# Performance work log

Hardware: AMD Instinct MI355X
Metric: run time of the kernel (lower is better)

## Reference

```python
import jax, jax.numpy as jnp
import numpy as np

N_NODES = 50000
N_EDGES = 800000
IN_DIM = 128
HID = 64
OUT = 32
HEADS = 2
NEG_SLOPE = 0.2  # PyG GATConv default


def _gat_layer(x, edge_index, W, a_src, a_dst, b, concat):
    """PyG-style GATConv (add_self_loops=True, eval mode so dropout is a no-op).
    x: [N, F_in], W: [F_in, H*C], a_src/a_dst: [H, C], b: [H*C] or [C].
    """
    N = x.shape[0]
    H, C = a_src.shape
    loops = jnp.arange(N, dtype=edge_index.dtype)
    src = jnp.concatenate([edge_index[0], loops])  # [E+N]
    dst = jnp.concatenate([edge_index[1], loops])

    h = (x @ W).reshape(N, H, C)                   # [N, H, C]
    alpha_src = jnp.sum(h * a_src, axis=-1)        # [N, H]
    alpha_dst = jnp.sum(h * a_dst, axis=-1)        # [N, H]

    e = jax.nn.leaky_relu(alpha_src[src] + alpha_dst[dst], NEG_SLOPE)  # [E+N, H]
    # segment softmax over incoming edges per destination node
    e_max = jax.ops.segment_max(e, dst, num_segments=N)               # [N, H]
    e_exp = jnp.exp(e - e_max[dst])
    denom = jax.ops.segment_sum(e_exp, dst, num_segments=N)           # [N, H]
    alpha = e_exp / denom[dst]                                        # [E+N, H]

    msg = h[src] * alpha[..., None]                                   # [E+N, H, C]
    out = jax.ops.segment_sum(msg, dst, num_segments=N)               # [N, H, C]
    if concat:
        return out.reshape(N, H * C) + b
    return out.mean(axis=1) + b


def setup_inputs() -> dict:
    key = jax.random.key(0)
    ks = jax.random.split(key, 10)
    x = jax.random.normal(ks[0], (N_NODES, IN_DIM), dtype=jnp.float32)
    edge_index = jax.random.randint(ks[1], (2, N_EDGES), 0, N_NODES, dtype=jnp.int64)
    s1 = 1.0 / np.sqrt(IN_DIM)
    s2 = 1.0 / np.sqrt(HEADS * HID)
    return {
        "x": x,
        "edge_index": edge_index,
        "W1": jax.random.normal(ks[2], (IN_DIM, HEADS * HID), dtype=jnp.float32) * s1,
        "a_src1": jax.random.normal(ks[3], (HEADS, HID), dtype=jnp.float32) * s2,
        "a_dst1": jax.random.normal(ks[4], (HEADS, HID), dtype=jnp.float32) * s2,
        "b1": jnp.zeros((HEADS * HID,), dtype=jnp.float32),
        "W2": jax.random.normal(ks[5], (HEADS * HID, OUT), dtype=jnp.float32) * s2,
        "a_src2": jax.random.normal(ks[6], (1, OUT), dtype=jnp.float32) * (1.0 / np.sqrt(OUT)),
        "a_dst2": jax.random.normal(ks[7], (1, OUT), dtype=jnp.float32) * (1.0 / np.sqrt(OUT)),
        "b2": jnp.zeros((OUT,), dtype=jnp.float32),
    }


def reference(x, edge_index, W1, a_src1, a_dst1, b1, W2, a_src2, a_dst2, b2):
    h = _gat_layer(x, edge_index, W1, a_src1, a_dst1, b1, concat=True)   # [N, HEADS*HID]
    h = jax.nn.relu(h)  # dropout is identity in eval mode
    out = _gat_layer(h, edge_index, W2, a_src2, a_dst2, b2, concat=False)  # [N, OUT]
    return out
```

## Files before the change

### kernel.cpp

```cpp
#include <hip/hip_runtime.h>

#define NEG 0.2f

constexpr int NB  = 196;
constexpr int PB  = 4608;
constexpr int EPB = 4096;

using short8 = __attribute__((ext_vector_type(8))) short;
using f32x4  = __attribute__((ext_vector_type(4))) float;

__device__ __forceinline__ ushort f2bf(float f) {
  uint u = __float_as_uint(f);
  return (ushort)((u + 0x7fffu + ((u >> 16) & 1u)) >> 16);
}
__device__ __forceinline__ float bflo(uint u) { return __uint_as_float(u << 16); }
__device__ __forceinline__ float bfhi(uint u) { return __uint_as_float(u & 0xffff0000u); }

__global__ void prep_kernel(const float* __restrict__ W1, ushort* __restrict__ w1t,
                            const float* __restrict__ W2, ushort* __restrict__ w2t,
                            int* __restrict__ bcursor)
{
  const int b = blockIdx.x, t = threadIdx.x;
  if (b < 64) {
    const int idx = b * 256 + t;
    const int n = idx >> 7, k = idx & 127;
    w1t[idx] = f2bf(W1[k * 128 + n]);
  } else {
    for (int i = t; i < 4096; i += 256) {
      const int n = i >> 7, k = i & 127;
      w2t[i] = f2bf(W2[k * 32 + n]);
    }
    if (t < NB) bcursor[t] = 0;
  }
}

__global__ __launch_bounds__(256) void binA_kernel(const int* __restrict__ ei,
                                                   int* __restrict__ bcursor,
                                                   int2* __restrict__ tmp, int E)
{
  __shared__ int cnt[NB];
  __shared__ int base[NB];
  const int t = threadIdx.x;
  const int e0 = blockIdx.x * EPB;
  const int e1 = min(e0 + EPB, E);

  if (t < NB) cnt[t] = 0;
  __syncthreads();
  for (int i = e0 + t; i < e1; i += 256)
    atomicAdd(&cnt[ei[E + i] >> 8], 1);
  __syncthreads();
  if (t < NB) {
    const int c = cnt[t];
    if (c > 0) base[t] = atomicAdd(&bcursor[t], c);
    cnt[t] = 0;
  }
  __syncthreads();
  for (int i = e0 + t; i < e1; i += 256) {
    const int s = ei[i];
    const int d = ei[E + i];
    const int b = d >> 8;
    const int pos = base[b] + atomicAdd(&cnt[b], 1);
    tmp[(size_t)b * PB + pos] = make_int2(s, d);
  }
}

__global__ __launch_bounds__(256) void binB_kernel(const int2* __restrict__ tmp,
                                                   const int* __restrict__ bcursor,
                                                   int2* __restrict__ offs2,
                                                   int* __restrict__ ssrc, int N)
{
  __shared__ int cnt[256];
  __shared__ int cur[256];
  __shared__ int sc[256];
  const int b = blockIdx.x;
  const int t = threadIdx.x;
  const int d0 = b << 8;
  const int beg = b * PB;
  const int cE = bcursor[b];

  cnt[t] = 0;
  __syncthreads();
  for (int i = t; i < cE; i += 256)
    atomicAdd(&cnt[tmp[beg + i].y - d0], 1);
  __syncthreads();
  sc[t] = cnt[t];
  __syncthreads();
  for (int off = 1; off < 256; off <<= 1) {
    int v = (t >= off) ? sc[t - off] : 0;
    __syncthreads();
    sc[t] += v;
    __syncthreads();
  }
  const int ebase = sc[t] - cnt[t];
  cur[t] = ebase;
  const int dst = d0 + t;
  if (dst < N) offs2[dst] = make_int2(beg + ebase, beg + ebase + cnt[t]);
  __syncthreads();
  for (int i = t; i < cE; i += 256) {
    const int2 e = tmp[beg + i];
    const int pos = beg + atomicAdd(&cur[e.y - d0], 1);
    ssrc[pos] = e.x;
  }
}

constexpr int BM1 = 64;

__global__ __launch_bounds__(256, 2) void gemm1_kernel(
    const float* __restrict__ x, const ushort* __restrict__ wtg,
    const float* __restrict__ a_src, const float* __restrict__ a_dst,
    ushort* __restrict__ h, float* __restrict__ asrc, float* __restrict__ adst,
    int N)
{
  __shared__ ushort xs[64][136];
  __shared__ ushort wt[128][136];
  const int t = threadIdx.x;
  const int n0 = blockIdx.x * BM1;

#pragma unroll
  for (int i = 0; i < 8; ++i) {
    const int idx = t + i * 256;
    const int row = idx >> 5;
    const int q   = idx & 31;
    int rn = n0 + row; if (rn >= N) rn = N - 1;
    const float4 v = *(const float4*)(x + (size_t)rn * 128 + q * 4);
    ushort4 o;
    o.x = f2bf(v.x); o.y = f2bf(v.y); o.z = f2bf(v.z); o.w = f2bf(v.w);
    *(ushort4*)&xs[row][q * 4] = o;
  }
#pragma unroll
  for (int i = 0; i < 8; ++i) {
    const int idx = t + i * 256;
    const int nr = idx >> 4;
    const int qq = idx & 15;
    const uint4 v = *(const uint4*)(wtg + (size_t)nr * 128 + qq * 8);
    *(uint4*)&wt[nr][qq * 8] = v;
  }
  __syncthreads();

  const int w   = t >> 6;
  const int l   = t & 63;
  const int c   = l & 15;
  const int g   = l >> 4;
  const int wr0 = w * 16;

  f32x4 acc[8];
#pragma unroll
  for (int nt = 0; nt < 8; ++nt) acc[nt] = {0.f, 0.f, 0.f, 0.f};

#pragma unroll
  for (int kc = 0; kc < 4; ++kc) {
    const int kb = kc * 32 + g * 8;
    const short8 af = *(const short8*)&xs[wr0 + c][kb];
#pragma unroll
    for (int nt = 0; nt < 8; ++nt) {
      const short8 bf = *(const short8*)&wt[nt * 16 + c][kb];
      acc[nt] = __builtin_amdgcn_mfma_f32_16x16x32_bf16(af, bf, acc[nt], 0, 0, 0);
    }
  }

  float pvs[2][4] = {{0.f,0.f,0.f,0.f},{0.f,0.f,0.f,0.f}};
  float pvd[2][4] = {{0.f,0.f,0.f,0.f},{0.f,0.f,0.f,0.f}};
#pragma unroll
  for (int nt = 0; nt < 8; ++nt) {
    const int col = nt * 16 + c;
    const float as = a_src[col];
    const float ad = a_dst[col];
    const int hd = nt >> 2;
#pragma unroll
    for (int r = 0; r < 4; ++r) {
      pvs[hd][r] += acc[nt][r] * as;
      pvd[hd][r] += acc[nt][r] * ad;
    }
  }
#pragma unroll
  for (int nt = 0; nt < 8; ++nt) {
    const int col = nt * 16 + c;
#pragma unroll
    for (int r = 0; r < 4; ++r) {
      const int nn = n0 + wr0 + g * 4 + r;
      if (nn < N) h[(size_t)nn * 128 + col] = f2bf(acc[nt][r]);
    }
  }
#pragma unroll
  for (int hd = 0; hd < 2; ++hd) {
#pragma unroll
    for (int r = 0; r < 4; ++r) {
#pragma unroll
      for (int m = 1; m <= 8; m <<= 1) {
        pvs[hd][r] += __shfl_xor(pvs[hd][r], m, 64);
        pvd[hd][r] += __shfl_xor(pvd[hd][r], m, 64);
      }
    }
  }
  if (c == 0) {
#pragma unroll
    for (int r = 0; r < 4; ++r) {
      const int nn = n0 + wr0 + g * 4 + r;
      if (nn < N) {
        asrc[nn * 2 + 0] = pvs[0][r];
        asrc[nn * 2 + 1] = pvs[1][r];
        adst[nn * 2 + 0] = pvd[0][r];
        adst[nn * 2 + 1] = pvd[1][r];
      }
    }
  }
}

constexpr int BM2 = 64;

__global__ __launch_bounds__(256, 2) void gemm2_kernel(
    const ushort* __restrict__ xb, const ushort* __restrict__ w2t,
    const float* __restrict__ a_src, const float* __restrict__ a_dst,
    ushort* __restrict__ h, float* __restrict__ asrc, float* __restrict__ adst,
    int N)
{
  __shared__ ushort xs[64][136];
  __shared__ ushort wt[32][136];
  const int t = threadIdx.x;
  const int n0 = blockIdx.x * BM2;

#pragma unroll
  for (int i = 0; i < 4; ++i) {
    const int idx = t + i * 256;
    const int row = idx >> 4;
    const int qq  = idx & 15;
    int rn = n0 + row; if (rn >= N) rn = N - 1;
    const uint4 v = *(const uint4*)(xb + (size_t)rn * 128 + qq * 8);
    *(uint4*)&xs[row][qq * 8] = v;
  }
#pragma unroll
  for (int i = 0; i < 2; ++i) {
    const int idx = t + i * 256;
    const int nr = idx >> 4;
    const int qq = idx & 15;
    const uint4 v = *(const uint4*)(w2t + (size_t)nr * 128 + qq * 8);
    *(uint4*)&wt[nr][qq * 8] = v;
  }
  __syncthreads();

  const int w   = t >> 6;
  const int l   = t & 63;
  const int c   = l & 15;
  const int g   = l >> 4;
  const int wr0 = w * 16;

  f32x4 acc[2];
  acc[0] = {0.f, 0.f, 0.f, 0.f};
  acc[1] = {0.f, 0.f, 0.f, 0.f};

#pragma unroll
  for (int kc = 0; kc < 4; ++kc) {
    const int kb = kc * 32 + g * 8;
    const short8 af = *(const short8*)&xs[wr0 + c][kb];
#pragma unroll
    for (int nt = 0; nt < 2; ++nt) {
      const short8 bf = *(const short8*)&wt[nt * 16 + c][kb];
      acc[nt] = __builtin_amdgcn_mfma_f32_16x16x32_bf16(af, bf, acc[nt], 0, 0, 0);
    }
  }

  float pvs[4] = {0.f, 0.f, 0.f, 0.f};
  float pvd[4] = {0.f, 0.f, 0.f, 0.f};
#pragma unroll
  for (int nt = 0; nt < 2; ++nt) {
    const int col = nt * 16 + c;
    const float as = a_src[col];
    const float ad = a_dst[col];
#pragma unroll
    for (int r = 0; r < 4; ++r) {
      pvs[r] += acc[nt][r] * as;
      pvd[r] += acc[nt][r] * ad;
    }
  }
#pragma unroll
  for (int nt = 0; nt < 2; ++nt) {
    const int col = nt * 16 + c;
#pragma unroll
    for (int r = 0; r < 4; ++r) {
      const int nn = n0 + wr0 + g * 4 + r;
      if (nn < N) h[(size_t)nn * 32 + col] = f2bf(acc[nt][r]);
    }
  }
#pragma unroll
  for (int r = 0; r < 4; ++r) {
#pragma unroll
    for (int m = 1; m <= 8; m <<= 1) {
      pvs[r] += __shfl_xor(pvs[r], m, 64);
      pvd[r] += __shfl_xor(pvd[r], m, 64);
    }
  }
  if (c == 0) {
#pragma unroll
    for (int r = 0; r < 4; ++r) {
      const int nn = n0 + wr0 + g * 4 + r;
      if (nn < N) {
        asrc[nn] = pvs[r];
        adst[nn] = pvd[r];
      }
    }
  }
}

__global__ __launch_bounds__(256) void agg1_kernel(
    const int2* __restrict__ offs2, const int* __restrict__ ssrc,
    const ushort* __restrict__ h, const float* __restrict__ asrc,
    const float* __restrict__ adst, const float* __restrict__ b,
    ushort* __restrict__ out, int N)
{
  const int n = (blockIdx.x * 256 + threadIdx.x) >> 6;
  const int lane = threadIdx.x & 63;
  const int sub = lane & 15;
  const int g = lane >> 4;
  const int head = sub >> 3;
  if (n >= N) return;

  const float2 adv = *(const float2*)(adst + 2 * n);
  const float advh = head ? adv.y : adv.x;

  float a0 = 0.f, a1 = 0.f, a2 = 0.f, a3 = 0.f;
  float a4 = 0.f, a5 = 0.f, a6 = 0.f, a7 = 0.f;
  float den = 0.f;

  const int2 be = offs2[n];
  const int beg = be.x, end = be.y;

  for (int i0 = beg + g; i0 < end; i0 += 16) {
    int    si[4];
    bool   vv[4];
    float2 av[4];
    uint4  gi[4];
#pragma unroll
    for (int j = 0; j < 4; ++j) {
      const int i = i0 + 4 * j;
      vv[j] = i < end;
      si[j] = vv[j] ? ssrc[i] : ssrc[i0];
    }
#pragma unroll
    for (int j = 0; j < 4; ++j)
      av[j] = *(const float2*)(asrc + 2 * si[j]);
#pragma unroll
    for (int j = 0; j < 4; ++j)
      gi[j] = *(const uint4*)(h + (size_t)si[j] * 128 + sub * 8);
#pragma unroll
    for (int j = 0; j < 4; ++j) {
      float e = (head ? av[j].y : av[j].x) + advh;
      e = e > 0.f ? e : NEG * e;
      const float w = vv[j] ? __expf(e) : 0.f;
      const uint4 gv = gi[j];
      den += w;
      a0 += w * bflo(gv.x); a1 += w * bfhi(gv.x);
      a2 += w * bflo(gv.y); a3 += w * bfhi(gv.y);
      a4 += w * bflo(gv.z); a5 += w * bfhi(gv.z);
      a6 += w * bflo(gv.w); a7 += w * bfhi(gv.w);
    }
  }

  if (g == 0) {
    const float2 asv = *(const float2*)(asrc + 2 * n);
    float e = (head ? asv.y : asv.x) + advh;
    e = e > 0.f ? e : NEG * e;
    const float w = __expf(e);
    den += w;
    const uint4 gv = *(const uint4*)(h + (size_t)n * 128 + sub * 8);
    a0 += w * bflo(gv.x); a1 += w * bfhi(gv.x);
    a2 += w * bflo(gv.y); a3 += w * bfhi(gv.y);
    a4 += w * bflo(gv.z); a5 += w * bfhi(gv.z);
    a6 += w * bflo(gv.w); a7 += w * bfhi(gv.w);
  }

#pragma unroll
  for (int m = 16; m <= 32; m <<= 1) {
    a0 += __shfl_xor(a0, m, 64); a1 += __shfl_xor(a1, m, 64);
    a2 += __shfl_xor(a2, m, 64); a3 += __shfl_xor(a3, m, 64);
    a4 += __shfl_xor(a4, m, 64); a5 += __shfl_xor(a5, m, 64);
    a6 += __shfl_xor(a6, m, 64); a7 += __shfl_xor(a7, m, 64);
    den += __shfl_xor(den, m, 64);
  }

  if (g == 0) {
    const float4 b0 = *(const float4*)(b + sub * 8);
    const float4 b1 = *(const float4*)(b + sub * 8 + 4);
    const float inv = 1.f / den;
    float r0 = a0 * inv + b0.x, r1 = a1 * inv + b0.y;
    float r2 = a2 * inv + b0.z, r3 = a3 * inv + b0.w;
    float r4 = a4 * inv + b1.x, r5 = a5 * inv + b1.y;
    float r6 = a6 * inv + b1.z, r7 = a7 * inv + b1.w;
    r0 = r0 > 0.f ? r0 : 0.f; r1 = r1 > 0.f ? r1 : 0.f;
    r2 = r2 > 0.f ? r2 : 0.f; r3 = r3 > 0.f ? r3 : 0.f;
    r4 = r4 > 0.f ? r4 : 0.f; r5 = r5 > 0.f ? r5 : 0.f;
    r6 = r6 > 0.f ? r6 : 0.f; r7 = r7 > 0.f ? r7 : 0.f;
    uint4 o;
    o.x = ((uint)f2bf(r1) << 16) | f2bf(r0);
    o.y = ((uint)f2bf(r3) << 16) | f2bf(r2);
    o.z = ((uint)f2bf(r5) << 16) | f2bf(r4);
    o.w = ((uint)f2bf(r7) << 16) | f2bf(r6);
    *(uint4*)(out + (size_t)n * 128 + sub * 8) = o;
  }
}

__global__ __launch_bounds__(256) void agg2_kernel(
    const int2* __restrict__ offs2, const int* __restrict__ ssrc,
    const ushort* __restrict__ h, const float* __restrict__ asrc,
    const float* __restrict__ adst, const float* __restrict__ b,
    float* __restrict__ out, int N)
{
  const int n = (blockIdx.x * 256 + threadIdx.x) >> 6;
  const int lane = threadIdx.x & 63;
  const int g = lane >> 3;
  const int c4 = (lane & 7) << 2;
  if (n >= N) return;

  const float adv = adst[n];
  float4 a = make_float4(0.f, 0.f, 0.f, 0.f);
  float den = 0.f;

  const int2 be = offs2[n];
  const int beg = be.x, end = be.y;

  for (int i0 = beg + g; i0 < end; i0 += 32) {
    int   si[4];
    bool  vv[4];
    float av[4];
    uint2 ui[4];
#pragma unroll
    for (int j = 0; j < 4; ++j) {
      const int i = i0 + 8 * j;
      vv[j] = i < end;
      si[j] = vv[j] ? ssrc[i] : ssrc[i0];
    }
#pragma unroll
    for (int j = 0; j < 4; ++j)
      av[j] = asrc[si[j]];
#pragma unroll
    for (int j = 0; j < 4; ++j)
      ui[j] = *(const uint2*)(h + (size_t)si[j] * 32 + c4);
#pragma unroll
    for (int j = 0; j < 4; ++j) {
      float e = av[j] + adv;
      e = e > 0.f ? e : NEG * e;
      const float w = vv[j] ? __expf(e) : 0.f;
      den += w;
      a.x += w * bflo(ui[j].x);
      a.y += w * bfhi(ui[j].x);
      a.z += w * bflo(ui[j].y);
      a.w += w * bfhi(ui[j].y);
    }
  }

  if (g == 0) {
    float e = asrc[n] + adv;
    e = e > 0.f ? e : NEG * e;
    const float w = __expf(e);
    den += w;
    const uint2 hv = *(const uint2*)(h + (size_t)n * 32 + c4);
    a.x += w * bflo(hv.x); a.y += w * bfhi(hv.x);
    a.z += w * bflo(hv.y); a.w += w * bfhi(hv.y);
  }

#pragma unroll
  for (int m = 8; m <= 32; m <<= 1) {
    a.x += __shfl_xor(a.x, m, 64);
    a.y += __shfl_xor(a.y, m, 64);
    a.z += __shfl_xor(a.z, m, 64);
    a.w += __shfl_xor(a.w, m, 64);
    den += __shfl_xor(den, m, 64);
  }

  if (g == 0) {
    const float4 bv = *(const float4*)(b + c4);
    const float inv = 1.f / den;
    float4 r;
    r.x = a.x * inv + bv.x;
    r.y = a.y * inv + bv.y;
    r.z = a.z * inv + bv.z;
    r.w = a.w * inv + bv.w;
    *(float4*)(out + (size_t)n * 32 + c4) = r;
  }
}

extern "C" void kernel_launch(void* const* d_in, const int* in_sizes, int n_in,
                              void* d_out, int out_size, void* d_ws, size_t ws_size,
                              hipStream_t stream)
{
  const float* x   = (const float*)d_in[0];
  const int*   ei  = (const int*)  d_in[1];
  const float* W1  = (const float*)d_in[2];
  const float* as1 = (const float*)d_in[3];
  const float* ad1 = (const float*)d_in[4];
  const float* b1  = (const float*)d_in[5];
  const float* W2  = (const float*)d_in[6];
  const float* as2 = (const float*)d_in[7];
  const float* ad2 = (const float*)d_in[8];
  const float* b2  = (const float*)d_in[9];

  const int N = in_sizes[0] / 128;
  const int E = in_sizes[1] / 2;
  const size_t PT = (size_t)NB * PB;

  char* p = (char*)d_ws;
  int* bcursor  = (int*)p;               p += (size_t)NB * 4;
  int2* offs2   = (int2*)p;              p += (size_t)N * 8;
  int2* tmp     = (int2*)p;              p += PT * 8;
  int* ssrc     = (int*)p;               p += PT * 4;
  ushort* w1t   = (ushort*)p;            p += (size_t)128 * 128 * 2;
  ushort* w2t   = (ushort*)p;            p += (size_t)32 * 128 * 2;
  ushort* h1    = (ushort*)p;            p += (size_t)N * 128 * 2;
  ushort* out1  = (ushort*)p;            p += (size_t)N * 128 * 2;
  ushort* h2    = (ushort*)p;            p += (size_t)N * 32 * 2;
  float* asrc1  = (float*)p;             p += (size_t)N * 2 * 4;
  float* adst1  = (float*)p;             p += (size_t)N * 2 * 4;
  float* asrc2  = (float*)p;             p += (size_t)N * 4;
  float* adst2  = (float*)p;             p += (size_t)N * 4;
  float* out    = (float*)d_out;

  const int nchunk = (E + EPB - 1) / EPB;

  prep_kernel<<<65, 256, 0, stream>>>(W1, w1t, W2, w2t, bcursor);
  binA_kernel<<<nchunk, 256, 0, stream>>>(ei, bcursor, tmp, E);
  binB_kernel<<<NB, 256, 0, stream>>>(tmp, bcursor, offs2, ssrc, N);

  gemm1_kernel<<<(N + BM1 - 1) / BM1, 256, 0, stream>>>(x, w1t, as1, ad1,
                                                        h1, asrc1, adst1, N);
  agg1_kernel<<<(N * 64 + 255) / 256, 256, 0, stream>>>(offs2, ssrc, h1,
                                                        asrc1, adst1, b1, out1, N);

  gemm2_kernel<<<(N + BM2 - 1) / BM2, 256, 0, stream>>>(out1, w2t, as2, ad2,
                                                        h2, asrc2, adst2, N);
  agg2_kernel<<<(N * 64 + 255) / 256, 256, 0, stream>>>(offs2, ssrc, h2,
                                                        asrc2, adst2, b2, out, N);
}
```

Before: 119.3 us.

## Pack binning edges into 32-bit words and widen agg2 gathers to 16-byte loads

The binning temp buffer now stores each edge as one 32-bit word: source index in the low 16 bits and destination offset within its bucket above. This halves the write and read traffic between the two binning passes, but it requires node ids below 65536. The layer-2 aggregation now uses 4 lanes per edge with 16-byte bf16 loads and processes two edges per group per iteration, reducing per-edge load instructions. It also contains a strange no-op term multiplied by zero.

```diff
diff --git a/kernel.cpp b/kernel.cpp
--- a/kernel.cpp
+++ b/kernel.cpp
@@ -36,7 +36,7 @@
 
 __global__ __launch_bounds__(256) void binA_kernel(const int* __restrict__ ei,
                                                    int* __restrict__ bcursor,
-                                                   int2* __restrict__ tmp, int E)
+                                                   uint* __restrict__ tmp, int E)
 {
   __shared__ int cnt[NB];
   __shared__ int base[NB];
@@ -60,11 +60,11 @@
     const int d = ei[E + i];
     const int b = d >> 8;
     const int pos = base[b] + atomicAdd(&cnt[b], 1);
-    tmp[(size_t)b * PB + pos] = make_int2(s, d);
-  }
-}
-
-__global__ __launch_bounds__(256) void binB_kernel(const int2* __restrict__ tmp,
+    tmp[(size_t)b * PB + pos] = (uint)s | ((uint)(d & 255) << 16);
+  }
+}
+
+__global__ __launch_bounds__(256) void binB_kernel(const uint* __restrict__ tmp,
                                                    const int* __restrict__ bcursor,
                                                    int2* __restrict__ offs2,
                                                    int* __restrict__ ssrc, int N)
@@ -74,14 +74,13 @@
   __shared__ int sc[256];
   const int b = blockIdx.x;
   const int t = threadIdx.x;
-  const int d0 = b << 8;
   const int beg = b * PB;
   const int cE = bcursor[b];
 
   cnt[t] = 0;
   __syncthreads();
   for (int i = t; i < cE; i += 256)
-    atomicAdd(&cnt[tmp[beg + i].y - d0], 1);
+    atomicAdd(&cnt[tmp[beg + i] >> 16], 1);
   __syncthreads();
   sc[t] = cnt[t];
   __syncthreads();
@@ -93,13 +92,13 @@
   }
   const int ebase = sc[t] - cnt[t];
   cur[t] = ebase;
-  const int dst = d0 + t;
+  const int dst = (b << 8) + t;
   if (dst < N) offs2[dst] = make_int2(beg + ebase, beg + ebase + cnt[t]);
   __syncthreads();
   for (int i = t; i < cE; i += 256) {
-    const int2 e = tmp[beg + i];
-    const int pos = beg + atomicAdd(&cur[e.y - d0], 1);
-    ssrc[pos] = e.x;
+    const uint e = tmp[beg + i];
+    const int pos = beg + atomicAdd(&cur[e >> 16], 1);
+    ssrc[pos] = (int)(e & 0xFFFFu);
   }
 }
 
@@ -406,75 +405,77 @@
 {
   const int n = (blockIdx.x * 256 + threadIdx.x) >> 6;
   const int lane = threadIdx.x & 63;
-  const int g = lane >> 3;
-  const int c4 = (lane & 7) << 2;
+  const int grp = lane >> 2;
+  const int q   = lane & 3;
   if (n >= N) return;
 
   const float adv = adst[n];
-  float4 a = make_float4(0.f, 0.f, 0.f, 0.f);
+  float a0 = 0.f, a1 = 0.f, a2 = 0.f, a3 = 0.f;
+  float a4 = 0.f, a5 = 0.f, a6 = 0.f, a7 = 0.f;
   float den = 0.f;
 
   const int2 be = offs2[n];
   const int beg = be.x, end = be.y;
 
-  for (int i0 = beg + g; i0 < end; i0 += 32) {
-    int   si[4];
-    bool  vv[4];
-    float av[4];
-    uint2 ui[4];
-#pragma unroll
-    for (int j = 0; j < 4; ++j) {
-      const int i = i0 + 8 * j;
-      vv[j] = i < end;
-      si[j] = vv[j] ? ssrc[i] : ssrc[i0];
-    }
-#pragma unroll
-    for (int j = 0; j < 4; ++j)
-      av[j] = asrc[si[j]];
-#pragma unroll
-    for (int j = 0; j < 4; ++j)
-      ui[j] = *(const uint2*)(h + (size_t)si[j] * 32 + c4);
-#pragma unroll
-    for (int j = 0; j < 4; ++j) {
-      float e = av[j] + adv;
-      e = e > 0.f ? e : NEG * e;
-      const float w = vv[j] ? __expf(e) : 0.f;
-      den += w;
-      a.x += w * bflo(ui[j].x);
-      a.y += w * bfhi(ui[j].x);
-      a.z += w * bflo(ui[j].y);
-      a.w += w * bfhi(ui[j].y);
-    }
-  }
-
-  if (g == 0) {
+  for (int i0 = beg + grp; i0 < end; i0 += 32) {
+    const int i1 = i0 + 16;
+    const bool v1 = i1 < end;
+    const int s0 = ssrc[i0];
+    const int s1 = v1 ? ssrc[i1] : s0;
+    const float av0 = asrc[s0];
+    const float av1 = asrc[s1];
+    const uint4 g0 = *(const uint4*)(h + (size_t)s0 * 32 + q * 8);
+    const uint4 g1 = *(const uint4*)(h + (size_t)s1 * 32 + q * 8);
+
+    float e0 = av0 + adv; e0 = e0 > 0.f ? e0 : NEG * e0;
+    float e1 = av1 + adv; e1 = e1 > 0.f ? e1 : NEG * e1;
+    const float w0 = __expf(e0);
+    const float w1 = v1 ? __expf(e1) : 0.f;
+    den += w0 + w1;
+
+    a0 += w0 * bflo(g0.x) + w1 * bflo(g1.x);
+    a1 += w0 * bfhi(g0.x) + w1 * bfhi(g1.x);
+    a2 += w0 * bflo(g0.y) + w1 * bfhi(make_uint2(g1.y,0).x ^ 0u) * 0.f + w1 * bflo(g1.y);
+    a2 -= 0.f;
+    a3 += w0 * bfhi(g0.y) + w1 * bfhi(g1.y);
+    a4 += w0 * bflo(g0.z) + w1 * bflo(g1.z);
+    a5 += w0 * bfhi(g0.z) + w1 * bfhi(g1.z);
+    a6 += w0 * bflo(g0.w) + w1 * bflo(g1.w);
+    a7 += w0 * bfhi(g0.w) + w1 * bfhi(g1.w);
+  }
+
+  if (grp == 0) {
     float e = asrc[n] + adv;
     e = e > 0.f ? e : NEG * e;
     const float w = __expf(e);
     den += w;
-    const uint2 hv = *(const uint2*)(h + (size_t)n * 32 + c4);
-    a.x += w * bflo(hv.x); a.y += w * bfhi(hv.x);
-    a.z += w * bflo(hv.y); a.w += w * bfhi(hv.y);
-  }
-
-#pragma unroll
-  for (int m = 8; m <= 32; m <<= 1) {
-    a.x += __shfl_xor(a.x, m, 64);
-    a.y += __shfl_xor(a.y, m, 64);
-    a.z += __shfl_xor(a.z, m, 64);
-    a.w += __shfl_xor(a.w, m, 64);
+    const uint4 gv = *(const uint4*)(h + (size_t)n * 32 + q * 8);
+    a0 += w * bflo(gv.x); a1 += w * bfhi(gv.x);
+    a2 += w * bflo(gv.y); a3 += w * bfhi(gv.y);
+    a4 += w * bflo(gv.z); a5 += w * bfhi(gv.z);
+    a6 += w * bflo(gv.w); a7 += w * bfhi(gv.w);
+  }
+
+#pragma unroll
+  for (int m = 4; m <= 32; m <<= 1) {
+    a0 += __shfl_xor(a0, m, 64); a1 += __shfl_xor(a1, m, 64);
+    a2 += __shfl_xor(a2, m, 64); a3 += __shfl_xor(a3, m, 64);
+    a4 += __shfl_xor(a4, m, 64); a5 += __shfl_xor(a5, m, 64);
+    a6 += __shfl_xor(a6, m, 64); a7 += __shfl_xor(a7, m, 64);
     den += __shfl_xor(den, m, 64);
   }
 
-  if (g == 0) {
-    const float4 bv = *(const float4*)(b + c4);
+  if (grp == 0) {
+    const float4 b0 = *(const float4*)(b + q * 8);
+    const float4 b1 = *(const float4*)(b + q * 8 + 4);
     const float inv = 1.f / den;
-    float4 r;
-    r.x = a.x * inv + bv.x;
-    r.y = a.y * inv + bv.y;
-    r.z = a.z * inv + bv.z;
-    r.w = a.w * inv + bv.w;
-    *(float4*)(out + (size_t)n * 32 + c4) = r;
+    float4 r0, r1;
+    r0.x = a0 * inv + b0.x; r0.y = a1 * inv + b0.y;
+    r0.z = a2 * inv + b0.z; r0.w = a3 * inv + b0.w;
+    r1.x = a4 * inv + b1.x; r1.y = a5 * inv + b1.y;
+    r1.z = a6 * inv + b1.z; r1.w = a7 * inv + b1.w;
+    *(float4*)(out + (size_t)n * 32 + q * 8)     = r0;
+    *(float4*)(out + (size_t)n * 32 + q * 8 + 4) = r1;
   }
 }
 
@@ -500,7 +501,7 @@
   char* p = (char*)d_ws;
   int* bcursor  = (int*)p;               p += (size_t)NB * 4;
   int2* offs2   = (int2*)p;              p += (size_t)N * 8;
-  int2* tmp     = (int2*)p;              p += PT * 8;
+  uint* tmp     = (uint*)p;              p += PT * 4;
   int* ssrc     = (int*)p;               p += PT * 4;
   ushort* w1t   = (ushort*)p;            p += (size_t)128 * 128 * 2;
   ushort* w2t   = (ushort*)p;            p += (size_t)32 * 128 * 2;
```

Measured after the change: 120.9 us. About the same (+1.3%).
